# Performance work log

Measured on AMD Instinct MI355X. Metric: run time of the kernel, lower is better.

## Reference

```python
import jax, jax.numpy as jnp
import numpy as np

N_NODES = 100000
N_EDGES = 3200000
IN_F = 256
OUT_F = 256


def setup_inputs() -> dict:
    key = jax.random.key(0)
    k1, k2, k3, k4, k5 = jax.random.split(key, 5)
    input_ = jax.random.normal(k1, (N_NODES, IN_F), dtype=jnp.float32)
    edge_src = jax.random.randint(k2, (N_EDGES,), 0, N_NODES, dtype=jnp.int64)
    edge_dst = jax.random.randint(k3, (N_EDGES,), 0, N_NODES, dtype=jnp.int64)
    edge_val = jax.random.uniform(k4, (N_EDGES,), dtype=jnp.float32)
    stdv = 1.0 / np.sqrt(OUT_F)
    weight = jax.random.uniform(k5, (IN_F, OUT_F), dtype=jnp.float32,
                                minval=-stdv, maxval=stdv)
    return {"input_": input_, "edge_src": edge_src, "edge_dst": edge_dst,
            "edge_val": edge_val, "weight": weight}


def reference(input_, edge_src, edge_dst, edge_val, weight):
    # neighbor = spmm(adj, input_): adj in COO form (dst, src, val)
    gathered = edge_val[:, None] * input_[edge_src]          # [E, F]
    neighbor = jax.ops.segment_sum(gathered, edge_dst,
                                   num_segments=N_NODES)     # [N, F]
    ft_input = input_ @ weight                               # [N, O]
    ft_neighbor = neighbor @ weight                          # [N, O]
    return jnp.concatenate([ft_input, ft_neighbor], axis=1)  # [N, 2*O]
```

## Files before the change

### kernel.cpp

```cpp
#include <hip/hip_runtime.h>

#define N_NODES 100000
#define N_EDGES 3200000
#define F 256

#define BM 128
#define BN 256
#define BK 32

#define SCAN_NB ((N_NODES + 255) / 256)
#define EDGE_NB (N_EDGES / 256)

typedef __attribute__((ext_vector_type(8))) short short8;
typedef __attribute__((ext_vector_type(4))) float f32x4;

__device__ inline unsigned short f2bf(float f) {
    unsigned int u = __float_as_uint(f);
    unsigned int r = (u + 0x7fffu + ((u >> 16) & 1u)) >> 16;
    return (unsigned short)r;
}

__device__ inline float bf2f(unsigned short b) {
    return __uint_as_float(((unsigned int)b) << 16);
}

__global__ void wt_kernel(const float* __restrict__ W, unsigned short* __restrict__ Wt) {
    int idx = blockIdx.x * 256 + threadIdx.x;
    int n = idx >> 8;
    int k = idx & 255;
    Wt[n * 256 + k] = f2bf(W[k * 256 + n]);
}

__global__ __launch_bounds__(256)
void rank_hist_kernel(const int* __restrict__ dst, int* __restrict__ counts,
                      unsigned short* __restrict__ rank) {
    const int e = blockIdx.x * 256 + threadIdx.x;
    rank[e] = (unsigned short)atomicAdd(&counts[dst[e]], 1);
}

__global__ __launch_bounds__(256)
void scan1_kernel(const int* __restrict__ counts, int* __restrict__ row_start,
                  int* __restrict__ partials) {
    __shared__ int s[256];
    const int t = threadIdx.x;
    const int i = blockIdx.x * 256 + t;
    int v = (i < N_NODES) ? counts[i] : 0;
    s[t] = v;
    __syncthreads();
#pragma unroll
    for (int off = 1; off < 256; off <<= 1) {
        int x = (t >= off) ? s[t - off] : 0;
        __syncthreads();
        if (t >= off) s[t] += x;
        __syncthreads();
    }
    if (i < N_NODES) row_start[i] = s[t] - v;
    if (t == 255) partials[blockIdx.x] = s[t];
}

__global__ __launch_bounds__(512)
void scan2_kernel(int* __restrict__ partials) {
    __shared__ int s[512];
    const int t = threadIdx.x;
    int v = (t < SCAN_NB) ? partials[t] : 0;
    s[t] = v;
    __syncthreads();
#pragma unroll
    for (int off = 1; off < 512; off <<= 1) {
        int x = (t >= off) ? s[t - off] : 0;
        __syncthreads();
        if (t >= off) s[t] += x;
        __syncthreads();
    }
    if (t < SCAN_NB) partials[t] = s[t] - v;
}

__global__ __launch_bounds__(256)
void scan3_kernel(int* __restrict__ row_start, const int* __restrict__ partials) {
    const int i = blockIdx.x * 256 + threadIdx.x;
    if (i < N_NODES)
        row_start[i] += partials[blockIdx.x];
    if (i == 0) row_start[N_NODES] = N_EDGES;
}

__global__ __launch_bounds__(256)
void fill_kernel(const int* __restrict__ src, const int* __restrict__ dst,
                 const float* __restrict__ val,
                 const int* __restrict__ row_start,
                 const unsigned short* __restrict__ rank,
                 int2* __restrict__ recs) {
    const int e = blockIdx.x * 256 + threadIdx.x;
    const int d = dst[e];
    const int pos = row_start[d] + (int)rank[e];
    recs[pos] = make_int2(src[e], __float_as_int(val[e]));
}

__global__ __launch_bounds__(256, 2)
void gemm_kernel(const float* __restrict__ A,
                 const unsigned short* __restrict__ Wt,
                 float* __restrict__ out,
                 unsigned short* __restrict__ ftb)
{
    __shared__ unsigned short As[BM * BK];
    __shared__ unsigned short Bs[BN * BK];

    const int tid   = threadIdx.x;
    const int lane  = tid & 63;
    const int wave  = tid >> 6;
    const int waveM = wave >> 1;
    const int waveN = wave & 1;
    const int rowBase = blockIdx.x * BM;

    f32x4 acc[4][8];
#pragma unroll
    for (int i = 0; i < 4; i++)
#pragma unroll
        for (int j = 0; j < 8; j++) acc[i][j] = (f32x4)0.0f;

    const int sr = tid >> 2;
    const int sk = (tid & 3) * 8;
    const int quad = lane >> 4;
    const int l16  = lane & 15;

    for (int kt = 0; kt < 8; kt++) {
        const int k0 = kt * BK;
#pragma unroll
        for (int p = 0; p < 2; p++) {
            const int r = p * 64 + sr;
            const int grow = rowBase + r;
            short8 av;
            if (grow < N_NODES) {
                const float4* pa = (const float4*)(A + (size_t)grow * 256 + k0 + sk);
                float4 f0 = pa[0];
                float4 f1 = pa[1];
                av[0] = (short)f2bf(f0.x); av[1] = (short)f2bf(f0.y);
                av[2] = (short)f2bf(f0.z); av[3] = (short)f2bf(f0.w);
                av[4] = (short)f2bf(f1.x); av[5] = (short)f2bf(f1.y);
                av[6] = (short)f2bf(f1.z); av[7] = (short)f2bf(f1.w);
            } else {
                av = (short8)0;
            }
            *(short8*)(&As[r * BK + sk]) = av;
        }
#pragma unroll
        for (int p = 0; p < 4; p++) {
            const int r = p * 64 + sr;
            const uint4 wv = *(const uint4*)(Wt + (size_t)r * 256 + k0 + sk);
            *(uint4*)(&Bs[r * BK + sk]) = wv;
        }
        __syncthreads();

        short8 af[4], bfr[8];
#pragma unroll
        for (int i = 0; i < 4; i++)
            af[i] = *(const short8*)(&As[(waveM * 64 + i * 16 + l16) * BK + quad * 8]);
#pragma unroll
        for (int j = 0; j < 8; j++)
            bfr[j] = *(const short8*)(&Bs[(waveN * 128 + j * 16 + l16) * BK + quad * 8]);
#pragma unroll
        for (int i = 0; i < 4; i++)
#pragma unroll
            for (int j = 0; j < 8; j++)
                acc[i][j] = __builtin_amdgcn_mfma_f32_16x16x32_bf16(
                    af[i], bfr[j], acc[i][j], 0, 0, 0);
        __syncthreads();
    }

    const int colBase = waveN * 128;
#pragma unroll
    for (int i = 0; i < 4; i++) {
        const int row0 = rowBase + waveM * 64 + i * 16 + quad * 4;
#pragma unroll
        for (int j = 0; j < 8; j++) {
            const int col = colBase + j * 16 + l16;
#pragma unroll
            for (int r = 0; r < 4; r++) {
                const int row = row0 + r;
                if (row < N_NODES) {
                    float v = acc[i][j][r];
                    out[(size_t)row * 512 + col] = v;
                    ftb[(size_t)row * 256 + col] = f2bf(v);
                }
            }
        }
    }
}

__global__ __launch_bounds__(256)
void gather_kernel(const int* __restrict__ row_start,
                   const int2* __restrict__ recs,
                   const unsigned short* __restrict__ ftb,
                   float* __restrict__ out)
{
    const int n = blockIdx.x * 4 + (threadIdx.x >> 6);
    if (n >= N_NODES) return;
    const int lane = threadIdx.x & 63;

    const int beg = row_start[n];
    const int end = row_start[n + 1];

    float ax = 0.f, ay = 0.f, az = 0.f, aw = 0.f;

    int e = beg;

    if (e + 7 < end) {
        int2 r[8];
#pragma unroll
        for (int q = 0; q < 8; q++) r[q] = recs[e + q];
        while (true) {
            const int en = e + 8;
            const bool moreN = (en + 7 < end);
            int2 rn[8];
            if (moreN) {
#pragma unroll
                for (int q = 0; q < 8; q++) rn[q] = recs[en + q];
            }
            ushort4 u[8];
#pragma unroll
            for (int q = 0; q < 8; q++)
                u[q] = *(const ushort4*)(ftb + (size_t)r[q].x * 256 + lane * 4);
#pragma unroll
            for (int q = 0; q < 8; q++) {
                const float v = __int_as_float(r[q].y);
                ax += v * bf2f(u[q].x); ay += v * bf2f(u[q].y);
                az += v * bf2f(u[q].z); aw += v * bf2f(u[q].w);
            }
            e = en;
            if (!moreN) break;
#pragma unroll
            for (int q = 0; q < 8; q++) r[q] = rn[q];
        }
    }

    for (; e + 3 < end; e += 4) {
        int2 r0 = recs[e];
        int2 r1 = recs[e + 1];
        int2 r2 = recs[e + 2];
        int2 r3 = recs[e + 3];
        ushort4 u0 = *(const ushort4*)(ftb + (size_t)r0.x * 256 + lane * 4);
        ushort4 u1 = *(const ushort4*)(ftb + (size_t)r1.x * 256 + lane * 4);
        ushort4 u2 = *(const ushort4*)(ftb + (size_t)r2.x * 256 + lane * 4);
        ushort4 u3 = *(const ushort4*)(ftb + (size_t)r3.x * 256 + lane * 4);
        const float v0 = __int_as_float(r0.y);
        const float v1 = __int_as_float(r1.y);
        const float v2 = __int_as_float(r2.y);
        const float v3 = __int_as_float(r3.y);
        ax += v0 * bf2f(u0.x); ay += v0 * bf2f(u0.y);
        az += v0 * bf2f(u0.z); aw += v0 * bf2f(u0.w);
        ax += v1 * bf2f(u1.x); ay += v1 * bf2f(u1.y);
        az += v1 * bf2f(u1.z); aw += v1 * bf2f(u1.w);
        ax += v2 * bf2f(u2.x); ay += v2 * bf2f(u2.y);
        az += v2 * bf2f(u2.z); aw += v2 * bf2f(u2.w);
        ax += v3 * bf2f(u3.x); ay += v3 * bf2f(u3.y);
        az += v3 * bf2f(u3.z); aw += v3 * bf2f(u3.w);
    }
    for (; e < end; e++) {
        int2 r0 = recs[e];
        ushort4 u0 = *(const ushort4*)(ftb + (size_t)r0.x * 256 + lane * 4);
        const float v0 = __int_as_float(r0.y);
        ax += v0 * bf2f(u0.x); ay += v0 * bf2f(u0.y);
        az += v0 * bf2f(u0.z); aw += v0 * bf2f(u0.w);
    }

    float4 res = make_float4(ax, ay, az, aw);
    *(float4*)(out + (size_t)n * 512 + 256 + lane * 4) = res;
}

extern "C" void kernel_launch(void* const* d_in, const int* in_sizes, int n_in,
                              void* d_out, int out_size, void* d_ws, size_t ws_size,
                              hipStream_t stream)
{
    const float* input = (const float*)d_in[0];
    const int*   esrc  = (const int*)d_in[1];
    const int*   edst  = (const int*)d_in[2];
    const float* eval  = (const float*)d_in[3];
    const float* W     = (const float*)d_in[4];
    float* out = (float*)d_out;

    char* ws = (char*)d_ws;
    unsigned short* Wt   = (unsigned short*)(ws);
    int* counts          = (int*)(ws + 131072);
    int* row_start       = (int*)(ws + 532480);
    unsigned short* rank = (unsigned short*)(ws + 933888);
    int* partials        = (int*)(ws + 7334912);
    int2* recs           = (int2*)(ws + 7337984);
    unsigned short* ftb  = (unsigned short*)(ws + 7337984 + (size_t)N_EDGES * 8);

    hipMemsetAsync(counts, 0, N_NODES * sizeof(int), stream);

    wt_kernel<<<256, 256, 0, stream>>>(W, Wt);
    rank_hist_kernel<<<EDGE_NB, 256, 0, stream>>>(edst, counts, rank);
    scan1_kernel<<<SCAN_NB, 256, 0, stream>>>(counts, row_start, partials);
    scan2_kernel<<<1, 512, 0, stream>>>(partials);
    scan3_kernel<<<SCAN_NB, 256, 0, stream>>>(row_start, partials);
    fill_kernel<<<EDGE_NB, 256, 0, stream>>>(esrc, edst, eval, row_start, rank, recs);

    dim3 g((N_NODES + BM - 1) / BM);
    gemm_kernel<<<g, 256, 0, stream>>>(input, Wt, out, ftb);

    gather_kernel<<<(N_NODES + 3) / 4, 256, 0, stream>>>(row_start, recs, ftb, out);
}
```

Measured before the change: 743.7 us.

## Vectorize edge kernels, halve GEMM row tile, swap MFMA operands for vector stores

The histogram and fill kernels now handle four edges per thread, using 128-bit loads of dst/src/val and 64-bit rank accesses to cut per-edge instruction and launch overhead. The GEMM row tile shrinks from 128 to 64, with occupancy raised to three blocks per SIMD, giving more blocks and less register pressure. The MFMA operands are swapped so each lane holds four consecutive columns of one row, letting the epilogue write float4 outputs and packed bf16 pairs instead of scalar stores. The smaller tile loads the weight panel into shared memory twice as often per output row.

```diff
diff --git a/kernel.cpp b/kernel.cpp
--- a/kernel.cpp
+++ b/kernel.cpp
@@ -4,12 +4,12 @@
 #define N_EDGES 3200000
 #define F 256
 
-#define BM 128
+#define BM 64
 #define BN 256
 #define BK 32
 
 #define SCAN_NB ((N_NODES + 255) / 256)
-#define EDGE_NB (N_EDGES / 256)
+#define EDGE_NB4 (N_EDGES / 1024)
 
 typedef __attribute__((ext_vector_type(8))) short short8;
 typedef __attribute__((ext_vector_type(4))) float f32x4;
@@ -34,8 +34,14 @@
 __global__ __launch_bounds__(256)
 void rank_hist_kernel(const int* __restrict__ dst, int* __restrict__ counts,
                       unsigned short* __restrict__ rank) {
-    const int e = blockIdx.x * 256 + threadIdx.x;
-    rank[e] = (unsigned short)atomicAdd(&counts[dst[e]], 1);
+    const int e0 = (blockIdx.x * 256 + threadIdx.x) * 4;
+    const int4 d = *(const int4*)(dst + e0);
+    ushort4 r;
+    r.x = (unsigned short)atomicAdd(&counts[d.x], 1);
+    r.y = (unsigned short)atomicAdd(&counts[d.y], 1);
+    r.z = (unsigned short)atomicAdd(&counts[d.z], 1);
+    r.w = (unsigned short)atomicAdd(&counts[d.w], 1);
+    *(ushort4*)(rank + e0) = r;
 }
 
 __global__ __launch_bounds__(256)
@@ -89,13 +95,18 @@
                  const int* __restrict__ row_start,
                  const unsigned short* __restrict__ rank,
                  int2* __restrict__ recs) {
-    const int e = blockIdx.x * 256 + threadIdx.x;
-    const int d = dst[e];
-    const int pos = row_start[d] + (int)rank[e];
-    recs[pos] = make_int2(src[e], __float_as_int(val[e]));
-}
-
-__global__ __launch_bounds__(256, 2)
+    const int e0 = (blockIdx.x * 256 + threadIdx.x) * 4;
+    const int4   s  = *(const int4*)(src + e0);
+    const int4   d  = *(const int4*)(dst + e0);
+    const float4 v  = *(const float4*)(val + e0);
+    const ushort4 rk = *(const ushort4*)(rank + e0);
+    recs[row_start[d.x] + (int)rk.x] = make_int2(s.x, __float_as_int(v.x));
+    recs[row_start[d.y] + (int)rk.y] = make_int2(s.y, __float_as_int(v.y));
+    recs[row_start[d.z] + (int)rk.z] = make_int2(s.z, __float_as_int(v.z));
+    recs[row_start[d.w] + (int)rk.w] = make_int2(s.w, __float_as_int(v.w));
+}
+
+__global__ __launch_bounds__(256, 3)
 void gemm_kernel(const float* __restrict__ A,
                  const unsigned short* __restrict__ Wt,
                  float* __restrict__ out,
@@ -111,9 +122,9 @@
     const int waveN = wave & 1;
     const int rowBase = blockIdx.x * BM;
 
-    f32x4 acc[4][8];
-#pragma unroll
-    for (int i = 0; i < 4; i++)
+    f32x4 acc[2][8];
+#pragma unroll
+    for (int i = 0; i < 2; i++)
 #pragma unroll
         for (int j = 0; j < 8; j++) acc[i][j] = (f32x4)0.0f;
 
@@ -124,10 +135,8 @@
 
     for (int kt = 0; kt < 8; kt++) {
         const int k0 = kt * BK;
-#pragma unroll
-        for (int p = 0; p < 2; p++) {
-            const int r = p * 64 + sr;
-            const int grow = rowBase + r;
+        {
+            const int grow = rowBase + sr;
             short8 av;
             if (grow < N_NODES) {
                 const float4* pa = (const float4*)(A + (size_t)grow * 256 + k0 + sk);
@@ -140,7 +149,7 @@
             } else {
                 av = (short8)0;
             }
-            *(short8*)(&As[r * BK + sk]) = av;
+            *(short8*)(&As[sr * BK + sk]) = av;
         }
 #pragma unroll
         for (int p = 0; p < 4; p++) {
@@ -150,37 +159,34 @@
         }
         __syncthreads();
 
-        short8 af[4], bfr[8];
-#pragma unroll
-        for (int i = 0; i < 4; i++)
-            af[i] = *(const short8*)(&As[(waveM * 64 + i * 16 + l16) * BK + quad * 8]);
+        short8 af[2], bfr[8];
+#pragma unroll
+        for (int i = 0; i < 2; i++)
+            af[i] = *(const short8*)(&As[(waveM * 32 + i * 16 + l16) * BK + quad * 8]);
 #pragma unroll
         for (int j = 0; j < 8; j++)
             bfr[j] = *(const short8*)(&Bs[(waveN * 128 + j * 16 + l16) * BK + quad * 8]);
 #pragma unroll
-        for (int i = 0; i < 4; i++)
+        for (int i = 0; i < 2; i++)
 #pragma unroll
             for (int j = 0; j < 8; j++)
                 acc[i][j] = __builtin_amdgcn_mfma_f32_16x16x32_bf16(
-                    af[i], bfr[j], acc[i][j], 0, 0, 0);
-        __syncthreads();
-    }
-
-    const int colBase = waveN * 128;
-#pragma unroll
-    for (int i = 0; i < 4; i++) {
-        const int row0 = rowBase + waveM * 64 + i * 16 + quad * 4;
-#pragma unroll
-        for (int j = 0; j < 8; j++) {
-            const int col = colBase + j * 16 + l16;
-#pragma unroll
-            for (int r = 0; r < 4; r++) {
-                const int row = row0 + r;
-                if (row < N_NODES) {
-                    float v = acc[i][j][r];
-                    out[(size_t)row * 512 + col] = v;
-                    ftb[(size_t)row * 256 + col] = f2bf(v);
-                }
+                    bfr[j], af[i], acc[i][j], 0, 0, 0);
+        __syncthreads();
+    }
+
+#pragma unroll
+    for (int i = 0; i < 2; i++) {
+        const int row = rowBase + waveM * 32 + i * 16 + l16;
+        if (row < N_NODES) {
+#pragma unroll
+            for (int j = 0; j < 8; j++) {
+                const int col = waveN * 128 + j * 16 + quad * 4;
+                f32x4 v = acc[i][j];
+                *(f32x4*)(out + (size_t)row * 512 + col) = v;
+                unsigned int p0 = ((unsigned int)f2bf(v[1]) << 16) | f2bf(v[0]);
+                unsigned int p1 = ((unsigned int)f2bf(v[3]) << 16) | f2bf(v[2]);
+                *(uint2*)(ftb + (size_t)row * 256 + col) = make_uint2(p0, p1);
             }
         }
     }
@@ -289,11 +295,11 @@
     hipMemsetAsync(counts, 0, N_NODES * sizeof(int), stream);
 
     wt_kernel<<<256, 256, 0, stream>>>(W, Wt);
-    rank_hist_kernel<<<EDGE_NB, 256, 0, stream>>>(edst, counts, rank);
+    rank_hist_kernel<<<EDGE_NB4, 256, 0, stream>>>(edst, counts, rank);
     scan1_kernel<<<SCAN_NB, 256, 0, stream>>>(counts, row_start, partials);
     scan2_kernel<<<1, 512, 0, stream>>>(partials);
     scan3_kernel<<<SCAN_NB, 256, 0, stream>>>(row_start, partials);
-    fill_kernel<<<EDGE_NB, 256, 0, stream>>>(esrc, edst, eval, row_start, rank, recs);
+    fill_kernel<<<EDGE_NB4, 256, 0, stream>>>(esrc, edst, eval, row_start, rank, recs);
 
     dim3 g((N_NODES + BM - 1) / BM);
     gemm_kernel<<<g, 256, 0, stream>>>(input, Wt, out, ftb);
```

After: 733.2 us. Within noise of the previous version (-1.4%).
